# Performance work log

Measured on AMD Instinct MI355X. Metric: run time of the kernel, lower is better.

## Reference

```python
import jax, jax.numpy as jnp
import numpy as np

B, S, D = 4, 2048, 1024
H = 16
DH = D // H  # 64
THETA = 10000.0


def setup_inputs() -> dict:
    key = jax.random.key(0)
    ks = jax.random.split(key, 7)
    scale = 1.0 / np.sqrt(D)
    return {
        "Q": jax.random.normal(ks[0], (B, S, D), dtype=jnp.float32),
        "K": jax.random.normal(ks[1], (B, S, D), dtype=jnp.float32),
        "V": jax.random.normal(ks[2], (B, S, D), dtype=jnp.float32),
        "Wq": jax.random.normal(ks[3], (D, D), dtype=jnp.float32) * scale,
        "Wk": jax.random.normal(ks[4], (D, D), dtype=jnp.float32) * scale,
        "Wv": jax.random.normal(ks[5], (D, D), dtype=jnp.float32) * scale,
        "Wo": jax.random.normal(ks[6], (D, D), dtype=jnp.float32) * scale,
    }


def _rope_tables(seq_len, d_head, theta, dtype):
    inv_freq = 1.0 / theta ** (jnp.arange(0, d_head, 2, dtype=jnp.float32) / d_head)
    ang = jnp.arange(seq_len, dtype=jnp.float32)[:, None] * inv_freq[None, :]  # [S, DH/2]
    return jnp.sin(ang).astype(dtype), jnp.cos(ang).astype(dtype)


def _apply_rope(x, sin, cos):
    # x: [B, H, S, DH]; sin/cos: [S, DH/2] broadcast over B,H
    x1 = x[..., 0::2]
    x2 = x[..., 1::2]
    x1r = x1 * cos - x2 * sin
    x2r = x1 * sin + x2 * cos
    return jnp.stack([x1r, x2r], axis=-1).reshape(x.shape)


def reference(Q, K, V, Wq, Wk, Wv, Wo):
    seq_len = Q.shape[-2]
    q = Q @ Wq.T
    k = K @ Wk.T
    v = V @ Wv.T

    def split(x):  # [B, S, D] -> [B, H, S, DH]
        return x.reshape(x.shape[0], seq_len, H, DH).transpose(0, 2, 1, 3)

    qh, kh, vh = split(q), split(k), split(v)

    sin, cos = _rope_tables(seq_len, DH, THETA, qh.dtype)
    qh = _apply_rope(qh, sin, cos)
    kh = _apply_rope(kh, sin, cos)

    # attention in fp32 (matches original cast)
    qf = qh.astype(jnp.float32)
    kf = kh.astype(jnp.float32)
    vf = vh.astype(jnp.float32)
    scale = 1.0 / np.sqrt(DH)
    scores = jnp.einsum('bhqd,bhkd->bhqk', qf, kf) * scale
    causal = jnp.tril(jnp.ones((seq_len, seq_len), dtype=bool))
    scores = jnp.where(causal, scores, -jnp.inf)
    attn = jax.nn.softmax(scores, axis=-1)
    out_h = jnp.einsum('bhqk,bhkd->bhqd', attn, vf).astype(Q.dtype)

    out = out_h.transpose(0, 2, 1, 3).reshape(Q.shape[0], seq_len, D)
    return out @ Wo.T
```

## Files before the change

kernel.cpp:

```cpp
#include <hip/hip_runtime.h>
#include <hip/hip_bf16.h>
#include <cmath>

#define B_ 4
#define S_ 2048
#define D_ 1024
#define H_ 16
#define DH_ 64

typedef __bf16 bf16_t;
typedef __bf16 bf16x8 __attribute__((ext_vector_type(8)));
typedef __bf16 bf16x4 __attribute__((ext_vector_type(4)));
typedef float f32x4 __attribute__((ext_vector_type(4)));

static __device__ __forceinline__ f32x4 mfma16(bf16x8 a, bf16x8 b, f32x4 c) {
    return __builtin_amdgcn_mfma_f32_16x16x32_bf16(a, b, c, 0, 0, 0);
}

static __device__ __forceinline__ float fast_exp2(float x) {
#if __has_builtin(__builtin_amdgcn_exp2f)
    return __builtin_amdgcn_exp2f(x);
#else
    float r; asm("v_exp_f32 %0, %1" : "=v"(r) : "v"(x)); return r;
#endif
}

static __device__ __forceinline__ void glds16(const bf16_t* g, void* l) {
    __builtin_amdgcn_global_load_lds(
        (const __attribute__((address_space(1))) unsigned int*)g,
        (__attribute__((address_space(3))) unsigned int*)l, 16, 0, 0);
}

__global__ void rope_table_kernel(float2* __restrict__ tab) {
    int idx = blockIdx.x * 256 + threadIdx.x;
    int s = idx >> 5, i = idx & 31;
    float inv = powf(10000.f, -(2.f * i) / 64.f);
    float ang = (float)s * inv;
    tab[idx] = make_float2(sinf(ang), cosf(ang));
}

__global__ __launch_bounds__(256)
void cvt_kernel(const float* __restrict__ src, bf16_t* __restrict__ dst) {
    int i = blockIdx.x * 256 + threadIdx.x;
    const float4* s = (const float4*)(src + (size_t)i * 8);
    float4 a = s[0], b = s[1];
    bf16x8 v = { (__bf16)a.x, (__bf16)a.y, (__bf16)a.z, (__bf16)a.w,
                 (__bf16)b.x, (__bf16)b.y, (__bf16)b.z, (__bf16)b.w };
    *(bf16x8*)(dst + (size_t)i * 8) = v;
}

__global__ __launch_bounds__(256)
void wcvt_kernel(const float* __restrict__ Wq, const float* __restrict__ Wk,
                 const float* __restrict__ Wv, const float* __restrict__ Wo,
                 bf16_t* __restrict__ dst) {
    int i = blockIdx.x * 256 + threadIdx.x;
    int t = i >> 17, j = i & 131071;
    const float* src = (t == 0) ? Wq : (t == 1) ? Wk : (t == 2) ? Wv : Wo;
    const float4* s = (const float4*)(src + (size_t)j * 8);
    float4 a = s[0], b = s[1];
    bf16x8 v = { (__bf16)a.x, (__bf16)a.y, (__bf16)a.z, (__bf16)a.w,
                 (__bf16)b.x, (__bf16)b.y, (__bf16)b.z, (__bf16)b.w };
    *(bf16x8*)(dst + (size_t)i * 8) = v;
}

template<int EPI>
__global__ __launch_bounds__(256)
void proj_kernel(const bf16_t* __restrict__ X, const bf16_t* __restrict__ W,
                 bf16_t* __restrict__ dst, const float2* __restrict__ tab)
{
    __shared__ bf16x8 lA[128 * 8];
    __shared__ bf16x8 lB[128 * 8];
    const int tid = threadIdx.x;
    const int gm0 = blockIdx.x * 128;
    const int gn0 = blockIdx.y * 128;
    const int wid = tid >> 6, lane = tid & 63;
    const int lr = lane & 15, lh = lane >> 4;
    const int wm = (wid >> 1) * 64, wn = (wid & 1) * 64;

    f32x4 acc[4][4] = {};

    for (int kt = 0; kt < D_ / 64; ++kt) {
        const int k0 = kt * 64;
        __syncthreads();
        #pragma unroll
        for (int i = 0; i < 4; ++i) {
            int base = wid * 64 + i * 256;
            int slot = base + lane;
            int row = slot >> 3, s = slot & 7, c = s ^ (row & 7);
            glds16(X + (size_t)(gm0 + row) * D_ + k0 + c * 8, &lA[base]);
            glds16(W + (size_t)(gn0 + row) * D_ + k0 + c * 8, &lB[base]);
        }
        __syncthreads();
        #pragma unroll
        for (int ks = 0; ks < 2; ++ks) {
            bf16x8 af[4], bfr[4];
            int kh = ks * 4 + lh;
            #pragma unroll
            for (int mi = 0; mi < 4; ++mi) { int r = wm + mi * 16 + lr; af[mi]  = lA[r * 8 + (kh ^ (r & 7))]; }
            #pragma unroll
            for (int ni = 0; ni < 4; ++ni) { int r = wn + ni * 16 + lr; bfr[ni] = lB[r * 8 + (kh ^ (r & 7))]; }
            #pragma unroll
            for (int mi = 0; mi < 4; ++mi)
                #pragma unroll
                for (int ni = 0; ni < 4; ++ni)
                    acc[mi][ni] = mfma16(af[mi], bfr[ni], acc[mi][ni]);
        }
    }

    #pragma unroll
    for (int mi = 0; mi < 4; ++mi) {
        #pragma unroll
        for (int j = 0; j < 4; ++j) {
            int m = gm0 + wm + mi * 16 + lh * 4 + j;
            int b = m >> 11, s = m & (S_ - 1);
            #pragma unroll
            for (int ni = 0; ni < 4; ++ni) {
                int n = gn0 + wn + ni * 16 + lr;
                int h = n >> 6, dh = n & 63;
                float x = acc[mi][ni][j];
                if (EPI == 0) {
                    float p = __shfl_xor(x, 1);
                    float2 sc = tab[s * 32 + (dh >> 1)];
                    float r = (dh & 1) ? (p * sc.x + x * sc.y)
                                       : (x * sc.y - p * sc.x);
                    dst[(((size_t)b * H_ + h) * S_ + s) * DH_ + dh] = (bf16_t)r;
                } else {
                    dst[(((size_t)b * H_ + h) * DH_ + dh) * S_ + s] = (bf16_t)x;
                }
            }
        }
    }
}

__global__ __launch_bounds__(512, 4)
void attn_kernel(const bf16_t* __restrict__ qh, const bf16_t* __restrict__ kh,
                 const bf16_t* __restrict__ vT, bf16_t* __restrict__ O)
{
    __shared__ bf16x8 lK[64 * 8];
    __shared__ bf16x8 lV[64 * 8];
    __shared__ bf16x8 lP8[8][128];
    const int tid = threadIdx.x, wid = tid >> 6, lane = tid & 63;
    const int lr = lane & 15, lh = lane >> 4;
    const int bh = blockIdx.x & 63;
    const int p  = blockIdx.x >> 6;
    const bf16_t* Qp = qh + (size_t)bh * S_ * DH_;
    const bf16_t* Kp = kh + (size_t)bh * S_ * DH_;
    const bf16_t* Vp = vT + (size_t)bh * DH_ * S_;
    char* lP = (char*)lP8[wid];
    const int b = bh >> 4, h = bh & 15;
    const float QSCALE = 0.125f * 1.44269504f;

    #pragma unroll 1
    for (int ph = 0; ph < 2; ++ph) {
        const int q0 = (ph == 0 ? (15 - p) : p) * 128;
        const int wq = q0 + wid * 16;

        bf16x8 qf[2];
        #pragma unroll
        for (int ks = 0; ks < 2; ++ks) {
            bf16x8 t = *(const bf16x8*)(Qp + (size_t)(wq + lr) * DH_ + ks * 32 + lh * 8);
            #pragma unroll
            for (int e = 0; e < 8; ++e) t[e] = (__bf16)((float)t[e] * QSCALE);
            qf[ks] = t;
        }

        f32x4 accO[4] = {};
        float mrun = -1e30f, lrun = 0.f;
        const int nkt = q0 / 64 + 2;

        #pragma unroll 1
        for (int kt = 0; kt < nkt; ++kt) {
            __syncthreads();
            {
                int slot = (wid << 6) + lane;
                int row = slot >> 3, s = slot & 7, c = s ^ (row & 7);
                glds16(Kp + (size_t)(kt * 64 + row) * DH_ + c * 8, &lK[wid << 6]);
                glds16(Vp + (size_t)row * S_ + kt * 64 + c * 8, &lV[wid << 6]);
            }
            __syncthreads();

            if (kt * 64 > wq + 15) continue;

            f32x4 sc[4] = {};
            __builtin_amdgcn_s_setprio(1);
            #pragma unroll
            for (int ks = 0; ks < 2; ++ks) {
                int kh8 = ks * 4 + lh;
                #pragma unroll
                for (int kvi = 0; kvi < 4; ++kvi) {
                    int r = kvi * 16 + lr;
                    bf16x8 kf = lK[r * 8 + (kh8 ^ (r & 7))];
                    sc[kvi] = mfma16(kf, qf[ks], sc[kvi]);
                }
            }
            __builtin_amdgcn_s_setprio(0);

            const bool needm = (kt * 64 + 63 > wq);
            const int kvb = kt * 64 + 4 * lh;
            const int qg = wq + lr;
            float pv[16];
            #pragma unroll
            for (int kvi = 0; kvi < 4; ++kvi)
                #pragma unroll
                for (int j = 0; j < 4; ++j) {
                    float x = sc[kvi][j];
                    if (needm && (kvb + kvi * 16 + j) > qg) x = -1e30f;
                    pv[kvi * 4 + j] = x;
                }
            float m8[8], m4v[4];
            #pragma unroll
            for (int i = 0; i < 8; ++i) m8[i] = fmaxf(pv[i], pv[i + 8]);
            #pragma unroll
            for (int i = 0; i < 4; ++i) m4v[i] = fmaxf(m8[i], m8[i + 4]);
            float mx = fmaxf(fmaxf(m4v[0], m4v[2]), fmaxf(m4v[1], m4v[3]));
            mx = fmaxf(mx, __shfl_xor(mx, 16));
            mx = fmaxf(mx, __shfl_xor(mx, 32));

            float mnew;
            float rs = 1.f;
            bool skip = __all(mx <= mrun + 8.0f);
            if (skip) {
                mnew = mrun;
            } else {
                mnew = fmaxf(mrun, mx);
                rs = fast_exp2(mrun - mnew);
                mrun = mnew;
            }
            #pragma unroll
            for (int i = 0; i < 16; ++i) pv[i] = fast_exp2(pv[i] - mnew);
            float s8[8], s4v[4];
            #pragma unroll
            for (int i = 0; i < 8; ++i) s8[i] = pv[i] + pv[i + 8];
            #pragma unroll
            for (int i = 0; i < 4; ++i) s4v[i] = s8[i] + s8[i + 4];
            float sum = (s4v[0] + s4v[1]) + (s4v[2] + s4v[3]);
            sum += __shfl_xor(sum, 16);
            sum += __shfl_xor(sum, 32);

            #pragma unroll
            for (int kvi = 0; kvi < 4; ++kvi) {
                bf16x4 hv = { (__bf16)pv[kvi * 4 + 0], (__bf16)pv[kvi * 4 + 1],
                              (__bf16)pv[kvi * 4 + 2], (__bf16)pv[kvi * 4 + 3] };
                int slot = 2 * kvi + (lh >> 1);
                *(bf16x4*)(lP + lr * 128 + ((slot ^ (lr & 7)) * 16) + (lh & 1) * 8) = hv;
            }

            if (skip) {
                lrun += sum;
            } else {
                lrun = lrun * rs + sum;
                #pragma unroll
                for (int j = 0; j < 4; ++j) {
                    float rj = __shfl(rs, 4 * lh + j);
                    #pragma unroll
                    for (int ni = 0; ni < 4; ++ni) accO[ni][j] *= rj;
                }
            }

            __builtin_amdgcn_s_setprio(1);
            #pragma unroll
            for (int ks = 0; ks < 2; ++ks) {
                int kh8 = ks * 4 + lh;
                int slot = 4 * ks + lh;
                bf16x8 pf = *(const bf16x8*)(lP + lr * 128 + ((slot ^ (lr & 7)) * 16));
                #pragma unroll
                for (int ni = 0; ni < 4; ++ni) {
                    int r = ni * 16 + lr;
                    bf16x8 vf = lV[r * 8 + (kh8 ^ (r & 7))];
                    accO[ni] = mfma16(pf, vf, accO[ni]);
                }
            }
            __builtin_amdgcn_s_setprio(0);
        }

        #pragma unroll
        for (int j = 0; j < 4; ++j) {
            int s = wq + 4 * lh + j;
            float inv = 1.f / __shfl(lrun, 4 * lh + j);
            #pragma unroll
            for (int ni = 0; ni < 4; ++ni) {
                int dh = ni * 16 + lr;
                O[((size_t)(b * S_ + s)) * D_ + h * DH_ + dh] = (bf16_t)(accO[ni][j] * inv);
            }
        }
    }
}

__global__ __launch_bounds__(256)
void out_kernel(const bf16_t* __restrict__ A, const bf16_t* __restrict__ W,
                float* __restrict__ out)
{
    __shared__ bf16x8 lA[128 * 8];
    __shared__ bf16x8 lB[128 * 8];
    const int tid = threadIdx.x;
    const int gm0 = blockIdx.x * 128;
    const int gn0 = blockIdx.y * 128;
    const int wid = tid >> 6, lane = tid & 63;
    const int lr = lane & 15, lh = lane >> 4;
    const int wm = (wid >> 1) * 64, wn = (wid & 1) * 64;

    f32x4 acc[4][4] = {};

    for (int kt = 0; kt < D_ / 64; ++kt) {
        const int k0 = kt * 64;
        __syncthreads();
        #pragma unroll
        for (int i = 0; i < 4; ++i) {
            int base = wid * 64 + i * 256;
            int slot = base + lane;
            int row = slot >> 3, s = slot & 7, c = s ^ (row & 7);
            glds16(A + (size_t)(gm0 + row) * D_ + k0 + c * 8, &lA[base]);
            glds16(W + (size_t)(gn0 + row) * D_ + k0 + c * 8, &lB[base]);
        }
        __syncthreads();
        #pragma unroll
        for (int ks = 0; ks < 2; ++ks) {
            bf16x8 af[4], bfr[4];
            int kh = ks * 4 + lh;
            #pragma unroll
            for (int mi = 0; mi < 4; ++mi) { int r = wm + mi * 16 + lr; af[mi]  = lA[r * 8 + (kh ^ (r & 7))]; }
            #pragma unroll
            for (int ni = 0; ni < 4; ++ni) { int r = wn + ni * 16 + lr; bfr[ni] = lB[r * 8 + (kh ^ (r & 7))]; }
            #pragma unroll
            for (int mi = 0; mi < 4; ++mi)
                #pragma unroll
                for (int ni = 0; ni < 4; ++ni)
                    acc[mi][ni] = mfma16(af[mi], bfr[ni], acc[mi][ni]);
        }
    }

    #pragma unroll
    for (int mi = 0; mi < 4; ++mi)
        #pragma unroll
        for (int j = 0; j < 4; ++j) {
            int m = gm0 + wm + mi * 16 + lh * 4 + j;
            #pragma unroll
            for (int ni = 0; ni < 4; ++ni) {
                int n = gn0 + wn + ni * 16 + lr;
                out[(size_t)m * D_ + n] = acc[mi][ni][j];
            }
        }
}

extern "C" void kernel_launch(void* const* d_in, const int* in_sizes, int n_in,
                              void* d_out, int out_size, void* d_ws, size_t ws_size,
                              hipStream_t stream)
{
    const float* Q  = (const float*)d_in[0];
    const float* K  = (const float*)d_in[1];
    const float* V  = (const float*)d_in[2];
    const float* Wq = (const float*)d_in[3];
    const float* Wk = (const float*)d_in[4];
    const float* Wv = (const float*)d_in[5];
    const float* Wo = (const float*)d_in[6];
    float* out = (float*)d_out;

    char* ws = (char*)d_ws;
    const size_t MB = 1024 * 1024;
    bf16_t* Xbf = (bf16_t*)(ws);
    bf16_t* Ob  = (bf16_t*)(ws);
    bf16_t* qh  = (bf16_t*)(ws + 16 * MB);
    bf16_t* khb = (bf16_t*)(ws + 32 * MB);
    bf16_t* vT  = (bf16_t*)(ws + 48 * MB);
    bf16_t* Wb  = (bf16_t*)(ws + 64 * MB);
    float2* tab = (float2*)(ws + 72 * MB);

    rope_table_kernel<<<S_ * 32 / 256, 256, 0, stream>>>(tab);
    wcvt_kernel<<<2048, 256, 0, stream>>>(Wq, Wk, Wv, Wo, Wb);

    dim3 g(64, 8);
    const int XBLK = (B_ * S_ * D_) / 8 / 256;

    cvt_kernel<<<XBLK, 256, 0, stream>>>(Q, Xbf);
    proj_kernel<0><<<g, 256, 0, stream>>>(Xbf, Wb + 0 * 1048576, qh, tab);
    cvt_kernel<<<XBLK, 256, 0, stream>>>(K, Xbf);
    proj_kernel<0><<<g, 256, 0, stream>>>(Xbf, Wb + 1 * 1048576, khb, tab);
    cvt_kernel<<<XBLK, 256, 0, stream>>>(V, Xbf);
    proj_kernel<1><<<g, 256, 0, stream>>>(Xbf, Wb + 2 * 1048576, vT, tab);

    attn_kernel<<<512, 512, 0, stream>>>(qh, khb, vT, Ob);

    out_kernel<<<g, 256, 0, stream>>>(Ob, Wb + 3 * 1048576, out);
}
```

Baseline: 205.7 us.

## Fuse input conversion into projections, batch QKV GEMMs, restructure attention grid

Merges the rope-table and weight-conversion kernels into one prep launch. Removes the separate fp32-to-bf16 activation conversion passes by loading fp32 inputs straight into LDS and converting while building MFMA fragments, and runs all three projections in one 3D-grid launch. Attention switches from 512-thread blocks that each handle two paired 128-row query tiles to 256-thread blocks that each handle one 64-row tile, launched heaviest first. This cuts launches and the round trip of activations through memory, in exchange for twice the fp32 LDS traffic in the projections and possible load imbalance in attention.

Result: slower. 213.3 us (+3.7%).

```diff
diff --git a/kernel.cpp b/kernel.cpp
--- a/kernel.cpp
+++ b/kernel.cpp
@@ -25,48 +25,276 @@
 #endif
 }
 
-static __device__ __forceinline__ void glds16(const bf16_t* g, void* l) {
+static __device__ __forceinline__ void glds16(const void* g, void* l) {
     __builtin_amdgcn_global_load_lds(
         (const __attribute__((address_space(1))) unsigned int*)g,
         (__attribute__((address_space(3))) unsigned int*)l, 16, 0, 0);
 }
 
-__global__ void rope_table_kernel(float2* __restrict__ tab) {
-    int idx = blockIdx.x * 256 + threadIdx.x;
-    int s = idx >> 5, i = idx & 31;
-    float inv = powf(10000.f, -(2.f * i) / 64.f);
-    float ang = (float)s * inv;
-    tab[idx] = make_float2(sinf(ang), cosf(ang));
-}
-
 __global__ __launch_bounds__(256)
-void cvt_kernel(const float* __restrict__ src, bf16_t* __restrict__ dst) {
-    int i = blockIdx.x * 256 + threadIdx.x;
-    const float4* s = (const float4*)(src + (size_t)i * 8);
-    float4 a = s[0], b = s[1];
-    bf16x8 v = { (__bf16)a.x, (__bf16)a.y, (__bf16)a.z, (__bf16)a.w,
-                 (__bf16)b.x, (__bf16)b.y, (__bf16)b.z, (__bf16)b.w };
-    *(bf16x8*)(dst + (size_t)i * 8) = v;
+void prep_kernel(const float* __restrict__ Wq, const float* __restrict__ Wk,
+                 const float* __restrict__ Wv, const float* __restrict__ Wo,
+                 bf16_t* __restrict__ Wb, float2* __restrict__ tab)
+{
+    int bid = blockIdx.x;
+    if (bid < 256) {
+        int idx = bid * 256 + threadIdx.x;
+        int s = idx >> 5, i = idx & 31;
+        float inv = powf(10000.f, -(2.f * i) / 64.f);
+        float ang = (float)s * inv;
+        tab[idx] = make_float2(sinf(ang), cosf(ang));
+    } else {
+        int i = (bid - 256) * 256 + threadIdx.x;
+        int t = i >> 17, j = i & 131071;
+        const float* src = (t == 0) ? Wq : (t == 1) ? Wk : (t == 2) ? Wv : Wo;
+        const float4* s = (const float4*)(src + (size_t)j * 8);
+        float4 a = s[0], b = s[1];
+        bf16x8 v = { (__bf16)a.x, (__bf16)a.y, (__bf16)a.z, (__bf16)a.w,
+                     (__bf16)b.x, (__bf16)b.y, (__bf16)b.z, (__bf16)b.w };
+        *(bf16x8*)(Wb + (size_t)i * 8) = v;
+    }
 }
 
 __global__ __launch_bounds__(256)
-void wcvt_kernel(const float* __restrict__ Wq, const float* __restrict__ Wk,
-                 const float* __restrict__ Wv, const float* __restrict__ Wo,
-                 bf16_t* __restrict__ dst) {
-    int i = blockIdx.x * 256 + threadIdx.x;
-    int t = i >> 17, j = i & 131071;
-    const float* src = (t == 0) ? Wq : (t == 1) ? Wk : (t == 2) ? Wv : Wo;
-    const float4* s = (const float4*)(src + (size_t)j * 8);
-    float4 a = s[0], b = s[1];
-    bf16x8 v = { (__bf16)a.x, (__bf16)a.y, (__bf16)a.z, (__bf16)a.w,
-                 (__bf16)b.x, (__bf16)b.y, (__bf16)b.z, (__bf16)b.w };
-    *(bf16x8*)(dst + (size_t)i * 8) = v;
-}
-
-template<int EPI>
+void proj3_kernel(const float* __restrict__ Qi, const float* __restrict__ Ki,
+                  const float* __restrict__ Vi, const bf16_t* __restrict__ Wb,
+                  bf16_t* __restrict__ qh, bf16_t* __restrict__ kh,
+                  bf16_t* __restrict__ vT, const float2* __restrict__ tab)
+{
+    __shared__ float4 lAf[128 * 16];
+    __shared__ bf16x8 lB[128 * 8];
+    const int z = blockIdx.z;
+    const float* X = (z == 0) ? Qi : (z == 1) ? Ki : Vi;
+    const bf16_t* W = Wb + (size_t)z * 1048576;
+    bf16_t* dst = (z == 0) ? qh : (z == 1) ? kh : vT;
+    const int epi = (z == 2) ? 1 : 0;
+
+    const int tid = threadIdx.x;
+    const int gm0 = blockIdx.x * 128;
+    const int gn0 = blockIdx.y * 128;
+    const int wid = tid >> 6, lane = tid & 63;
+    const int lr = lane & 15, lh = lane >> 4;
+    const int wm = (wid >> 1) * 64, wn = (wid & 1) * 64;
+
+    f32x4 acc[4][4] = {};
+
+    for (int kt = 0; kt < D_ / 64; ++kt) {
+        const int k0 = kt * 64;
+        __syncthreads();
+        #pragma unroll
+        for (int i = 0; i < 8; ++i) {
+            int base = i * 256 + wid * 64;
+            int slot = base + lane;
+            int row = slot >> 4, s = slot & 15, c = s ^ (row & 15);
+            glds16(X + (size_t)(gm0 + row) * D_ + k0 + c * 4, &lAf[base]);
+        }
+        #pragma unroll
+        for (int i = 0; i < 4; ++i) {
+            int base = i * 256 + wid * 64;
+            int slot = base + lane;
+            int row = slot >> 3, s = slot & 7, c = s ^ (row & 7);
+            glds16(W + (size_t)(gn0 + row) * D_ + k0 + c * 8, &lB[base]);
+        }
+        __syncthreads();
+        #pragma unroll
+        for (int ks = 0; ks < 2; ++ks) {
+            int kh8 = ks * 4 + lh;
+            bf16x8 af[4], bfr[4];
+            #pragma unroll
+            for (int mi = 0; mi < 4; ++mi) {
+                int r = wm + mi * 16 + lr;
+                float4 a0 = lAf[r * 16 + ((2 * kh8) ^ (r & 15))];
+                float4 a1 = lAf[r * 16 + ((2 * kh8 + 1) ^ (r & 15))];
+                af[mi] = bf16x8{ (__bf16)a0.x, (__bf16)a0.y, (__bf16)a0.z, (__bf16)a0.w,
+                                 (__bf16)a1.x, (__bf16)a1.y, (__bf16)a1.z, (__bf16)a1.w };
+            }
+            #pragma unroll
+            for (int ni = 0; ni < 4; ++ni) { int r = wn + ni * 16 + lr; bfr[ni] = lB[r * 8 + (kh8 ^ (r & 7))]; }
+            #pragma unroll
+            for (int mi = 0; mi < 4; ++mi)
+                #pragma unroll
+                for (int ni = 0; ni < 4; ++ni)
+                    acc[mi][ni] = mfma16(af[mi], bfr[ni], acc[mi][ni]);
+        }
+    }
+
+    #pragma unroll
+    for (int mi = 0; mi < 4; ++mi) {
+        #pragma unroll
+        for (int j = 0; j < 4; ++j) {
+            int m = gm0 + wm + mi * 16 + lh * 4 + j;
+            int b = m >> 11, s = m & (S_ - 1);
+            #pragma unroll
+            for (int ni = 0; ni < 4; ++ni) {
+                int n = gn0 + wn + ni * 16 + lr;
+                int h = n >> 6, dh = n & 63;
+                float x = acc[mi][ni][j];
+                if (epi == 0) {
+                    float p = __shfl_xor(x, 1);
+                    float2 sc = tab[s * 32 + (dh >> 1)];
+                    float r = (dh & 1) ? (p * sc.x + x * sc.y)
+                                       : (x * sc.y - p * sc.x);
+                    dst[(((size_t)b * H_ + h) * S_ + s) * DH_ + dh] = (bf16_t)r;
+                } else {
+                    dst[(((size_t)b * H_ + h) * DH_ + dh) * S_ + s] = (bf16_t)x;
+                }
+            }
+        }
+    }
+}
+
+__global__ __launch_bounds__(256, 6)
+void attn_kernel(const bf16_t* __restrict__ qh, const bf16_t* __restrict__ kh,
+                 const bf16_t* __restrict__ vT, bf16_t* __restrict__ O)
+{
+    __shared__ bf16x8 lK[64 * 8];
+    __shared__ bf16x8 lV[64 * 8];
+    __shared__ bf16x8 lP8[4][128];
+    const int tid = threadIdx.x, wid = tid >> 6, lane = tid & 63;
+    const int lr = lane & 15, lh = lane >> 4;
+    const int bh = blockIdx.x & 63;
+    const int t  = 31 - (blockIdx.x >> 6);
+    const bf16_t* Qp = qh + (size_t)bh * S_ * DH_;
+    const bf16_t* Kp = kh + (size_t)bh * S_ * DH_;
+    const bf16_t* Vp = vT + (size_t)bh * DH_ * S_;
+    char* lP = (char*)lP8[wid];
+    const int b = bh >> 4, h = bh & 15;
+    const float QSCALE = 0.125f * 1.44269504f;
+    const int wq = t * 64 + wid * 16;
+
+    bf16x8 qf[2];
+    #pragma unroll
+    for (int ks = 0; ks < 2; ++ks) {
+        bf16x8 q8 = *(const bf16x8*)(Qp + (size_t)(wq + lr) * DH_ + ks * 32 + lh * 8);
+        #pragma unroll
+        for (int e = 0; e < 8; ++e) q8[e] = (__bf16)((float)q8[e] * QSCALE);
+        qf[ks] = q8;
+    }
+
+    f32x4 accO[4] = {};
+    float mrun = -1e30f, lrun = 0.f;
+    const int nkt = t + 1;
+
+    #pragma unroll 1
+    for (int kt = 0; kt < nkt; ++kt) {
+        __syncthreads();
+        #pragma unroll
+        for (int i = 0; i < 2; ++i) {
+            int base = i * 256 + (wid << 6);
+            int slot = base + lane;
+            int row = slot >> 3, s = slot & 7, c = s ^ (row & 7);
+            glds16(Kp + (size_t)(kt * 64 + row) * DH_ + c * 8, &lK[base]);
+            glds16(Vp + (size_t)row * S_ + kt * 64 + c * 8, &lV[base]);
+        }
+        __syncthreads();
+
+        f32x4 sc[4] = {};
+        __builtin_amdgcn_s_setprio(1);
+        #pragma unroll
+        for (int ks = 0; ks < 2; ++ks) {
+            int kh8 = ks * 4 + lh;
+            #pragma unroll
+            for (int kvi = 0; kvi < 4; ++kvi) {
+                int r = kvi * 16 + lr;
+                bf16x8 kf = lK[r * 8 + (kh8 ^ (r & 7))];
+                sc[kvi] = mfma16(kf, qf[ks], sc[kvi]);
+            }
+        }
+        __builtin_amdgcn_s_setprio(0);
+
+        const bool needm = (kt == t);
+        const int kvb = kt * 64 + 4 * lh;
+        const int qg = wq + lr;
+        float pv[16];
+        #pragma unroll
+        for (int kvi = 0; kvi < 4; ++kvi)
+            #pragma unroll
+            for (int j = 0; j < 4; ++j) {
+                float x = sc[kvi][j];
+                if (needm && (kvb + kvi * 16 + j) > qg) x = -1e30f;
+                pv[kvi * 4 + j] = x;
+            }
+        float m8[8], m4v[4];
+        #pragma unroll
+        for (int i = 0; i < 8; ++i) m8[i] = fmaxf(pv[i], pv[i + 8]);
+        #pragma unroll
+        for (int i = 0; i < 4; ++i) m4v[i] = fmaxf(m8[i], m8[i + 4]);
+        float mx = fmaxf(fmaxf(m4v[0], m4v[2]), fmaxf(m4v[1], m4v[3]));
+        mx = fmaxf(mx, __shfl_xor(mx, 16));
+        mx = fmaxf(mx, __shfl_xor(mx, 32));
+
+        float mnew;
+        float rs = 1.f;
+        bool skip = __all(mx <= mrun + 8.0f);
+        if (skip) {
+            mnew = mrun;
+        } else {
+            mnew = fmaxf(mrun, mx);
+            rs = fast_exp2(mrun - mnew);
+            mrun = mnew;
+        }
+        #pragma unroll
+        for (int i = 0; i < 16; ++i) pv[i] = fast_exp2(pv[i] - mnew);
+        float s8[8], s4v[4];
+        #pragma unroll
+        for (int i = 0; i < 8; ++i) s8[i] = pv[i] + pv[i + 8];
+        #pragma unroll
+        for (int i = 0; i < 4; ++i) s4v[i] = s8[i] + s8[i + 4];
+        float sum = (s4v[0] + s4v[1]) + (s4v[2] + s4v[3]);
+        sum += __shfl_xor(sum, 16);
+        sum += __shfl_xor(sum, 32);
+
+        #pragma unroll
+        for (int kvi = 0; kvi < 4; ++kvi) {
+            bf16x4 hv = { (__bf16)pv[kvi * 4 + 0], (__bf16)pv[kvi * 4 + 1],
+                          (__bf16)pv[kvi * 4 + 2], (__bf16)pv[kvi * 4 + 3] };
+            int slot = 2 * kvi + (lh >> 1);
+            *(bf16x4*)(lP + lr * 128 + ((slot ^ (lr & 7)) * 16) + (lh & 1) * 8) = hv;
+        }
+
+        if (skip) {
+            lrun += sum;
+        } else {
+            lrun = lrun * rs + sum;
+            #pragma unroll
+            for (int j = 0; j < 4; ++j) {
+                float rj = __shfl(rs, 4 * lh + j);
+                #pragma unroll
+                for (int ni = 0; ni < 4; ++ni) accO[ni][j] *= rj;
+            }
+        }
+
+        __builtin_amdgcn_s_setprio(1);
+        #pragma unroll
+        for (int ks = 0; ks < 2; ++ks) {
+            int kh8 = ks * 4 + lh;
+            int slot = 4 * ks + lh;
+            bf16x8 pf = *(const bf16x8*)(lP + lr * 128 + ((slot ^ (lr & 7)) * 16));
+            #pragma unroll
+            for (int ni = 0; ni < 4; ++ni) {
+                int r = ni * 16 + lr;
+                bf16x8 vf = lV[r * 8 + (kh8 ^ (r & 7))];
+                accO[ni] = mfma16(pf, vf, accO[ni]);
+            }
+        }
+        __builtin_amdgcn_s_setprio(0);
+    }
+
+    #pragma unroll
+    for (int j = 0; j < 4; ++j) {
+        int s = wq + 4 * lh + j;
+        float inv = 1.f / __shfl(lrun, 4 * lh + j);
+        #pragma unroll
+        for (int ni = 0; ni < 4; ++ni) {
+            int dh = ni * 16 + lr;
+            O[((size_t)(b * S_ + s)) * D_ + h * DH_ + dh] = (bf16_t)(accO[ni][j] * inv);
+        }
+    }
+}
+
 __global__ __launch_bounds__(256)
-void proj_kernel(const bf16_t* __restrict__ X, const bf16_t* __restrict__ W,
-                 bf16_t* __restrict__ dst, const float2* __restrict__ tab)
+void out_kernel(const bf16_t* __restrict__ A, const bf16_t* __restrict__ W,
+                float* __restrict__ out)
 {
     __shared__ bf16x8 lA[128 * 8];
     __shared__ bf16x8 lB[128 * 8];
@@ -87,228 +315,6 @@
             int base = wid * 64 + i * 256;
             int slot = base + lane;
             int row = slot >> 3, s = slot & 7, c = s ^ (row & 7);
-            glds16(X + (size_t)(gm0 + row) * D_ + k0 + c * 8, &lA[base]);
-            glds16(W + (size_t)(gn0 + row) * D_ + k0 + c * 8, &lB[base]);
-        }
-        __syncthreads();
-        #pragma unroll
-        for (int ks = 0; ks < 2; ++ks) {
-            bf16x8 af[4], bfr[4];
-            int kh = ks * 4 + lh;
-            #pragma unroll
-            for (int mi = 0; mi < 4; ++mi) { int r = wm + mi * 16 + lr; af[mi]  = lA[r * 8 + (kh ^ (r & 7))]; }
-            #pragma unroll
-            for (int ni = 0; ni < 4; ++ni) { int r = wn + ni * 16 + lr; bfr[ni] = lB[r * 8 + (kh ^ (r & 7))]; }
-            #pragma unroll
-            for (int mi = 0; mi < 4; ++mi)
-                #pragma unroll
-                for (int ni = 0; ni < 4; ++ni)
-                    acc[mi][ni] = mfma16(af[mi], bfr[ni], acc[mi][ni]);
-        }
-    }
-
-    #pragma unroll
-    for (int mi = 0; mi < 4; ++mi) {
-        #pragma unroll
-        for (int j = 0; j < 4; ++j) {
-            int m = gm0 + wm + mi * 16 + lh * 4 + j;
-            int b = m >> 11, s = m & (S_ - 1);
-            #pragma unroll
-            for (int ni = 0; ni < 4; ++ni) {
-                int n = gn0 + wn + ni * 16 + lr;
-                int h = n >> 6, dh = n & 63;
-                float x = acc[mi][ni][j];
-                if (EPI == 0) {
-                    float p = __shfl_xor(x, 1);
-                    float2 sc = tab[s * 32 + (dh >> 1)];
-                    float r = (dh & 1) ? (p * sc.x + x * sc.y)
-                                       : (x * sc.y - p * sc.x);
-                    dst[(((size_t)b * H_ + h) * S_ + s) * DH_ + dh] = (bf16_t)r;
-                } else {
-                    dst[(((size_t)b * H_ + h) * DH_ + dh) * S_ + s] = (bf16_t)x;
-                }
-            }
-        }
-    }
-}
-
-__global__ __launch_bounds__(512, 4)
-void attn_kernel(const bf16_t* __restrict__ qh, const bf16_t* __restrict__ kh,
-                 const bf16_t* __restrict__ vT, bf16_t* __restrict__ O)
-{
-    __shared__ bf16x8 lK[64 * 8];
-    __shared__ bf16x8 lV[64 * 8];
-    __shared__ bf16x8 lP8[8][128];
-    const int tid = threadIdx.x, wid = tid >> 6, lane = tid & 63;
-    const int lr = lane & 15, lh = lane >> 4;
-    const int bh = blockIdx.x & 63;
-    const int p  = blockIdx.x >> 6;
-    const bf16_t* Qp = qh + (size_t)bh * S_ * DH_;
-    const bf16_t* Kp = kh + (size_t)bh * S_ * DH_;
-    const bf16_t* Vp = vT + (size_t)bh * DH_ * S_;
-    char* lP = (char*)lP8[wid];
-    const int b = bh >> 4, h = bh & 15;
-    const float QSCALE = 0.125f * 1.44269504f;
-
-    #pragma unroll 1
-    for (int ph = 0; ph < 2; ++ph) {
-        const int q0 = (ph == 0 ? (15 - p) : p) * 128;
-        const int wq = q0 + wid * 16;
-
-        bf16x8 qf[2];
-        #pragma unroll
-        for (int ks = 0; ks < 2; ++ks) {
-            bf16x8 t = *(const bf16x8*)(Qp + (size_t)(wq + lr) * DH_ + ks * 32 + lh * 8);
-            #pragma unroll
-            for (int e = 0; e < 8; ++e) t[e] = (__bf16)((float)t[e] * QSCALE);
-            qf[ks] = t;
-        }
-
-        f32x4 accO[4] = {};
-        float mrun = -1e30f, lrun = 0.f;
-        const int nkt = q0 / 64 + 2;
-
-        #pragma unroll 1
-        for (int kt = 0; kt < nkt; ++kt) {
-            __syncthreads();
-            {
-                int slot = (wid << 6) + lane;
-                int row = slot >> 3, s = slot & 7, c = s ^ (row & 7);
-                glds16(Kp + (size_t)(kt * 64 + row) * DH_ + c * 8, &lK[wid << 6]);
-                glds16(Vp + (size_t)row * S_ + kt * 64 + c * 8, &lV[wid << 6]);
-            }
-            __syncthreads();
-
-            if (kt * 64 > wq + 15) continue;
-
-            f32x4 sc[4] = {};
-            __builtin_amdgcn_s_setprio(1);
-            #pragma unroll
-            for (int ks = 0; ks < 2; ++ks) {
-                int kh8 = ks * 4 + lh;
-                #pragma unroll
-                for (int kvi = 0; kvi < 4; ++kvi) {
-                    int r = kvi * 16 + lr;
-                    bf16x8 kf = lK[r * 8 + (kh8 ^ (r & 7))];
-                    sc[kvi] = mfma16(kf, qf[ks], sc[kvi]);
-                }
-            }
-            __builtin_amdgcn_s_setprio(0);
-
-            const bool needm = (kt * 64 + 63 > wq);
-            const int kvb = kt * 64 + 4 * lh;
-            const int qg = wq + lr;
-            float pv[16];
-            #pragma unroll
-            for (int kvi = 0; kvi < 4; ++kvi)
-                #pragma unroll
-                for (int j = 0; j < 4; ++j) {
-                    float x = sc[kvi][j];
-                    if (needm && (kvb + kvi * 16 + j) > qg) x = -1e30f;
-                    pv[kvi * 4 + j] = x;
-                }
-            float m8[8], m4v[4];
-            #pragma unroll
-            for (int i = 0; i < 8; ++i) m8[i] = fmaxf(pv[i], pv[i + 8]);
-            #pragma unroll
-            for (int i = 0; i < 4; ++i) m4v[i] = fmaxf(m8[i], m8[i + 4]);
-            float mx = fmaxf(fmaxf(m4v[0], m4v[2]), fmaxf(m4v[1], m4v[3]));
-            mx = fmaxf(mx, __shfl_xor(mx, 16));
-            mx = fmaxf(mx, __shfl_xor(mx, 32));
-
-            float mnew;
-            float rs = 1.f;
-            bool skip = __all(mx <= mrun + 8.0f);
-            if (skip) {
-                mnew = mrun;
-            } else {
-                mnew = fmaxf(mrun, mx);
-                rs = fast_exp2(mrun - mnew);
-                mrun = mnew;
-            }
-            #pragma unroll
-            for (int i = 0; i < 16; ++i) pv[i] = fast_exp2(pv[i] - mnew);
-            float s8[8], s4v[4];
-            #pragma unroll
-            for (int i = 0; i < 8; ++i) s8[i] = pv[i] + pv[i + 8];
-            #pragma unroll
-            for (int i = 0; i < 4; ++i) s4v[i] = s8[i] + s8[i + 4];
-            float sum = (s4v[0] + s4v[1]) + (s4v[2] + s4v[3]);
-            sum += __shfl_xor(sum, 16);
-            sum += __shfl_xor(sum, 32);
-
-            #pragma unroll
-            for (int kvi = 0; kvi < 4; ++kvi) {
-                bf16x4 hv = { (__bf16)pv[kvi * 4 + 0], (__bf16)pv[kvi * 4 + 1],
-                              (__bf16)pv[kvi * 4 + 2], (__bf16)pv[kvi * 4 + 3] };
-                int slot = 2 * kvi + (lh >> 1);
-                *(bf16x4*)(lP + lr * 128 + ((slot ^ (lr & 7)) * 16) + (lh & 1) * 8) = hv;
-            }
-
-            if (skip) {
-                lrun += sum;
-            } else {
-                lrun = lrun * rs + sum;
-                #pragma unroll
-                for (int j = 0; j < 4; ++j) {
-                    float rj = __shfl(rs, 4 * lh + j);
-                    #pragma unroll
-                    for (int ni = 0; ni < 4; ++ni) accO[ni][j] *= rj;
-                }
-            }
-
-            __builtin_amdgcn_s_setprio(1);
-            #pragma unroll
-            for (int ks = 0; ks < 2; ++ks) {
-                int kh8 = ks * 4 + lh;
-                int slot = 4 * ks + lh;
-                bf16x8 pf = *(const bf16x8*)(lP + lr * 128 + ((slot ^ (lr & 7)) * 16));
-                #pragma unroll
-                for (int ni = 0; ni < 4; ++ni) {
-                    int r = ni * 16 + lr;
-                    bf16x8 vf = lV[r * 8 + (kh8 ^ (r & 7))];
-                    accO[ni] = mfma16(pf, vf, accO[ni]);
-                }
-            }
-            __builtin_amdgcn_s_setprio(0);
-        }
-
-        #pragma unroll
-        for (int j = 0; j < 4; ++j) {
-            int s = wq + 4 * lh + j;
-            float inv = 1.f / __shfl(lrun, 4 * lh + j);
-            #pragma unroll
-            for (int ni = 0; ni < 4; ++ni) {
-                int dh = ni * 16 + lr;
-                O[((size_t)(b * S_ + s)) * D_ + h * DH_ + dh] = (bf16_t)(accO[ni][j] * inv);
-            }
-        }
-    }
-}
-
-__global__ __launch_bounds__(256)
-void out_kernel(const bf16_t* __restrict__ A, const bf16_t* __restrict__ W,
-                float* __restrict__ out)
-{
-    __shared__ bf16x8 lA[128 * 8];
-    __shared__ bf16x8 lB[128 * 8];
-    const int tid = threadIdx.x;
-    const int gm0 = blockIdx.x * 128;
-    const int gn0 = blockIdx.y * 128;
-    const int wid = tid >> 6, lane = tid & 63;
-    const int lr = lane & 15, lh = lane >> 4;
-    const int wm = (wid >> 1) * 64, wn = (wid & 1) * 64;
-
-    f32x4 acc[4][4] = {};
-
-    for (int kt = 0; kt < D_ / 64; ++kt) {
-        const int k0 = kt * 64;
-        __syncthreads();
-        #pragma unroll
-        for (int i = 0; i < 4; ++i) {
-            int base = wid * 64 + i * 256;
-            int slot = base + lane;
-            int row = slot >> 3, s = slot & 7, c = s ^ (row & 7);
             glds16(A + (size_t)(gm0 + row) * D_ + k0 + c * 8, &lA[base]);
             glds16(W + (size_t)(gn0 + row) * D_ + k0 + c * 8, &lB[base]);
         }
@@ -357,7 +363,6 @@
 
     char* ws = (char*)d_ws;
     const size_t MB = 1024 * 1024;
-    bf16_t* Xbf = (bf16_t*)(ws);
     bf16_t* Ob  = (bf16_t*)(ws);
     bf16_t* qh  = (bf16_t*)(ws + 16 * MB);
     bf16_t* khb = (bf16_t*)(ws + 32 * MB);
@@ -365,20 +370,8 @@
     bf16_t* Wb  = (bf16_t*)(ws + 64 * MB);
     float2* tab = (float2*)(ws + 72 * MB);
 
-    rope_table_kernel<<<S_ * 32 / 256, 256, 0, stream>>>(tab);
-    wcvt_kernel<<<2048, 256, 0, stream>>>(Wq, Wk, Wv, Wo, Wb);
-
-    dim3 g(64, 8);
-    const int XBLK = (B_ * S_ * D_) / 8 / 256;
-
-    cvt_kernel<<<XBLK, 256, 0, stream>>>(Q, Xbf);
-    proj_kernel<0><<<g, 256, 0, stream>>>(Xbf, Wb + 0 * 1048576, qh, tab);
-    cvt_kernel<<<XBLK, 256, 0, stream>>>(K, Xbf);
-    proj_kernel<0><<<g, 256, 0, stream>>>(Xbf, Wb + 1 * 1048576, khb, tab);
-    cvt_kernel<<<XBLK, 256, 0, stream>>>(V, Xbf);
-    proj_kernel<1><<<g, 256, 0, stream>>>(Xbf, Wb + 2 * 1048576, vT, tab);
-
-    attn_kernel<<<512, 512, 0, stream>>>(qh, khb, vT, Ob);
-
-    out_kernel<<<g, 256, 0, stream>>>(Ob, Wb + 3 * 1048576, out);
-}
+    prep_kernel<<<2304, 256, 0, stream>>>(Wq, Wk, Wv, Wo, Wb, tab);
+    proj3_kernel<<<dim3(64, 8, 3), 256, 0, stream>>>(Q, K, V, Wb, qh, khb, vT, tab);
+    attn_kernel<<<2048, 256, 0, stream>>>(qh, khb, vT, Ob);
+    out_kernel<<<dim3(64, 8), 256, 0, stream>>>(Ob, Wb + 3 * 1048576, out);
+}
```
